# Optimization experiments

Measured on AMD Instinct MI355X. Metric: run time of the kernel, lower is better.

The kernel has to match this reference:

```python
import jax, jax.numpy as jnp
import numpy as np

N = 50000      # nodes
E = 800000     # edges (avg degree 16)
LM = 768       # lm_input_dim
H = 192        # hidden_dim = 32*6
B6 = 32        # per-branch dim = hidden_dim/6
SLOPE = 0.01   # nn.LeakyReLU default negative slope


def setup_inputs() -> dict:
    key = jax.random.key(0)
    ks = jax.random.split(key, 32)
    f = lambda i, shape, s=0.05: (jax.random.normal(ks[i], shape, jnp.float32) * s)
    inp = {
        "pre_x": f(0, (N, LM)),
        "x": f(1, (N, LM)),
        "edge_index": jax.random.randint(ks[2], (2, E), 0, N),
        "edge_type": jax.random.randint(ks[3], (E,), 0, 3),
        "num_prop": f(4, (N, 5)),
        "num_category": f(5, (N, 1)),
        "des_tensor": f(6, (N, LM)),
        "tweet_tensor": f(7, (N, LM)),
        # parameters (torch nn.Linear convention: W is [out, in], y = x @ W.T + b)
        "W_des": f(8, (B6, LM)), "b_des": f(9, (B6,)),
        "W_tweet": f(10, (B6, LM)), "b_tweet": f(11, (B6,)),
        "W_tweet_tr": f(12, (B6, LM)), "b_tweet_tr": f(13, (B6,)),
        "W_prop": f(14, (B6, 5)), "b_prop": f(15, (B6,)),
        "W_cat": f(16, (B6, 1)), "b_cat": f(17, (B6,)),
        "W_text": f(18, (B6, LM)), "b_text": f(19, (B6,)),
        "W_in": f(20, (H, H)), "b_in": f(21, (H,)),
        "W_c1": f(22, (H, H)), "b_c1": f(23, (H,)),
        "W_c2": f(24, (H, H)), "b_c2": f(25, (H,)),
        "W_o1": f(26, (96, H)), "b_o1": f(27, (96,)),
        "W_o2": f(28, (2, 96)), "b_o2": f(29, (2,)),
    }
    return inp


def _gcn_conv(h, W, b, src, dst):
    """PyG GCNConv: symmetric-normalized aggregation with added self-loops.
    out[v] = sum_{u->v} (d_u d_v)^{-1/2} (h_u W^T) + (1/d_v) (h_v W^T) + b
    where d includes the self-loop (+1)."""
    n = h.shape[0]
    hW = h @ W.T                                                  # [N, H]
    deg = jax.ops.segment_sum(jnp.ones(src.shape[0], h.dtype), dst,
                              num_segments=n) + 1.0               # [N]
    dinv = jax.lax.rsqrt(deg)
    norm = dinv[src] * dinv[dst]                                  # [E]
    agg = jax.ops.segment_sum(hW[src] * norm[:, None], dst,
                              num_segments=n)                     # [N, H]
    return agg + hW * (1.0 / deg)[:, None] + b


def reference(pre_x, x, edge_index, edge_type, num_prop, num_category,
              des_tensor, tweet_tensor,
              W_des, b_des, W_tweet, b_tweet, W_tweet_tr, b_tweet_tr,
              W_prop, b_prop, W_cat, b_cat, W_text, b_text,
              W_in, b_in, W_c1, b_c1, W_c2, b_c2,
              W_o1, b_o1, W_o2, b_o2):
    lrelu = lambda v: jax.nn.leaky_relu(v, SLOPE)
    branch = lambda t, W, b: lrelu(t @ W.T + b)   # dropout is identity in eval

    d = branch(des_tensor, W_des, b_des)
    pre_t = branch(pre_x, W_tweet, b_tweet)
    t = branch(x, W_tweet_tr, b_tweet_tr)
    n = branch(num_prop, W_prop, b_prop)
    c = branch(num_category, W_cat, b_cat)
    tw = branch(tweet_tensor, W_text, b_text)

    h = jnp.concatenate((n, c, d, tw, pre_t, t), axis=1)          # [N, 192]
    h = lrelu(h @ W_in.T + b_in)

    src, dst = edge_index[0], edge_index[1]
    h = _gcn_conv(h, W_c1, b_c1, src, dst)
    h = _gcn_conv(h, W_c2, b_c2, src, dst)

    em = lrelu(h @ W_o1.T + b_o1)                                 # [N, 96]
    out = em @ W_o2.T + b_o2                                      # [N, 2]
    return (out, em)
```

## Files before the change

kernel.cpp:

```cpp
#include <hip/hip_runtime.h>

#define NN 50000
#define EE 800000
#define LMD 768
#define HD 192
#define SLOPE 0.01f

typedef short bf16x8 __attribute__((ext_vector_type(8)));
typedef float f32x4 __attribute__((ext_vector_type(4)));
typedef unsigned short u16;

__device__ __forceinline__ float lrelu(float v){ return v > 0.f ? v : SLOPE * v; }

__device__ __forceinline__ u16 f2bf(float f){
    unsigned u = __float_as_uint(f);
    u += 0x7FFF + ((u >> 16) & 1u);
    return (u16)(u >> 16);
}
__device__ __forceinline__ float bf2f(u16 v){
    return __uint_as_float(((unsigned)v) << 16);
}

__global__ __launch_bounds__(256) void k_prep(
    const float* __restrict__ W0, const float* __restrict__ W1,
    const float* __restrict__ W2, const float* __restrict__ W3,
    const float* __restrict__ Win, const float* __restrict__ Wc1,
    const float* __restrict__ Wc2, const float* __restrict__ Wo1,
    u16* __restrict__ out)
{
    int m = blockIdx.y;
    int idx = blockIdx.x * 256 + threadIdx.x;
    const float* src; int nelem; int K;
    switch (m) {
      case 0: src = W0;  nelem = 32*768;  K = 768; break;
      case 1: src = W1;  nelem = 32*768;  K = 768; break;
      case 2: src = W2;  nelem = 32*768;  K = 768; break;
      case 3: src = W3;  nelem = 32*768;  K = 768; break;
      case 4: src = Win; nelem = 192*192; K = 192; break;
      case 5: src = Wc1; nelem = 192*192; K = 192; break;
      case 6: src = Wc2; nelem = 192*192; K = 192; break;
      default: src = Wo1; nelem = 96*192; K = 192; break;
    }
    if (idx >= nelem) return;
    u16 v = f2bf(src[idx]);
    int c = idx / K, k = idx - c * K;
    int cb = c >> 4, lr = c & 15;
    int sg = k >> 5, kk = k & 31, hi = kk >> 3, j = kk & 7;
    int lane = hi * 16 + lr;
    size_t dst;
    if (m < 4)      dst = (size_t)m * 24576 + (sg * 2 + cb) * 512 + lane * 8 + j;
    else if (m < 7) dst = 98304 + (size_t)(m - 4) * 36864 + (sg * 12 + cb) * 512 + lane * 8 + j;
    else            dst = 208896 + (size_t)(sg * 6 + cb) * 512 + lane * 8 + j;
    out[dst] = v;
}

__global__ __launch_bounds__(256) void k_branch(
    const float* __restrict__ des, const float* __restrict__ twt,
    const float* __restrict__ prex, const float* __restrict__ xx,
    const u16* __restrict__ Wf,
    const float* __restrict__ bd, const float* __restrict__ btx,
    const float* __restrict__ btw, const float* __restrict__ btr,
    u16* __restrict__ h)
{
    const int br = blockIdx.y;
    const float* A; const float* bias; int colBase;
    switch (br) {
      case 0:  A = des;  bias = bd;  colBase = 64;  break;
      case 1:  A = twt;  bias = btx; colBase = 96;  break;
      case 2:  A = prex; bias = btw; colBase = 128; break;
      default: A = xx;   bias = btr; colBase = 160; break;
    }
    const u16* Wb = Wf + br * 24576;

    const int t = threadIdx.x, w = t >> 6, l = t & 63;
    const int hi = l >> 4, lr = l & 15;
    const int rowBase = blockIdx.x * 64;
    int row = rowBase + w * 16 + lr;
    int rowc = row < NN ? row : NN - 1;
    const float4* ap = reinterpret_cast<const float4*>(A) + (size_t)rowc * 192;
    const int fo = hi * 2;

    f32x4 acc[2] = {};
    float4 buf[4][2];
    #pragma unroll
    for (int s = 0; s < 4; ++s) {
        buf[s][0] = ap[s * 8 + fo];
        buf[s][1] = ap[s * 8 + fo + 1];
    }

    #pragma unroll
    for (int sg = 0; sg < 24; ++sg) {
        float4 a0 = buf[sg & 3][0], a1 = buf[sg & 3][1];
        if (sg + 4 < 24) {
            buf[sg & 3][0] = ap[(sg + 4) * 8 + fo];
            buf[sg & 3][1] = ap[(sg + 4) * 8 + fo + 1];
        }
        bf16x8 af;
        af[0] = (short)f2bf(a0.x); af[1] = (short)f2bf(a0.y);
        af[2] = (short)f2bf(a0.z); af[3] = (short)f2bf(a0.w);
        af[4] = (short)f2bf(a1.x); af[5] = (short)f2bf(a1.y);
        af[6] = (short)f2bf(a1.z); af[7] = (short)f2bf(a1.w);
        #pragma unroll
        for (int cb = 0; cb < 2; ++cb) {
            bf16x8 bf = *reinterpret_cast<const bf16x8*>(Wb + (sg * 2 + cb) * 512 + l * 8);
            acc[cb] = __builtin_amdgcn_mfma_f32_16x16x32_bf16(af, bf, acc[cb], 0, 0, 0);
        }
    }

    #pragma unroll
    for (int cb = 0; cb < 2; ++cb) {
        int cl = cb * 16 + lr;
        float bv = bias[cl];
        #pragma unroll
        for (int rg = 0; rg < 4; ++rg) {
            int r = rowBase + w * 16 + hi * 4 + rg;
            if (r < NN)
                h[(size_t)r * HD + colBase + cl] = f2bf(lrelu(acc[cb][rg] + bv));
        }
    }
}

template<bool BIAS, bool LRELU>
__global__ __launch_bounds__(256) void k_hgemm(
    const u16* __restrict__ A, const u16* __restrict__ Wf,
    const float* __restrict__ bias, u16* __restrict__ out)
{
    const int t = threadIdx.x, w = t >> 6, l = t & 63;
    const int hi = l >> 4, lr = l & 15;
    const int rowBase = blockIdx.x * 64;
    int row = rowBase + w * 16 + lr;
    int rowc = row < NN ? row : NN - 1;
    const u16* ap = A + (size_t)rowc * HD;

    bf16x8 afr[6];
    #pragma unroll
    for (int sg = 0; sg < 6; ++sg)
        afr[sg] = *reinterpret_cast<const bf16x8*>(ap + sg * 32 + hi * 8);

    f32x4 acc[12] = {};
    #pragma unroll
    for (int sg = 0; sg < 6; ++sg) {
        #pragma unroll
        for (int cb = 0; cb < 12; ++cb) {
            bf16x8 bf = *reinterpret_cast<const bf16x8*>(Wf + (sg * 12 + cb) * 512 + l * 8);
            acc[cb] = __builtin_amdgcn_mfma_f32_16x16x32_bf16(afr[sg], bf, acc[cb], 0, 0, 0);
        }
    }

    #pragma unroll
    for (int cb = 0; cb < 12; ++cb) {
        int cl = cb * 16 + lr;
        float bv = BIAS ? bias[cl] : 0.f;
        #pragma unroll
        for (int rg = 0; rg < 4; ++rg) {
            int r = rowBase + w * 16 + hi * 4 + rg;
            if (r < NN) {
                float v = acc[cb][rg] + bv;
                if (LRELU) v = lrelu(v);
                out[(size_t)r * HD + cl] = f2bf(v);
            }
        }
    }
}

__global__ __launch_bounds__(256) void k_final(
    const u16* __restrict__ A, const u16* __restrict__ Wf,
    const float* __restrict__ b1, const float* __restrict__ W2,
    const float* __restrict__ b2, float* __restrict__ em, float* __restrict__ out)
{
    const int t = threadIdx.x, w = t >> 6, l = t & 63;
    const int hi = l >> 4, lr = l & 15;
    const int rowBase = blockIdx.x * 64;
    int row = rowBase + w * 16 + lr;
    int rowc = row < NN ? row : NN - 1;
    const u16* ap = A + (size_t)rowc * HD;

    bf16x8 afr[6];
    #pragma unroll
    for (int sg = 0; sg < 6; ++sg)
        afr[sg] = *reinterpret_cast<const bf16x8*>(ap + sg * 32 + hi * 8);

    f32x4 acc[6] = {};
    #pragma unroll
    for (int sg = 0; sg < 6; ++sg) {
        #pragma unroll
        for (int cb = 0; cb < 6; ++cb) {
            bf16x8 bf = *reinterpret_cast<const bf16x8*>(Wf + (sg * 6 + cb) * 512 + l * 8);
            acc[cb] = __builtin_amdgcn_mfma_f32_16x16x32_bf16(afr[sg], bf, acc[cb], 0, 0, 0);
        }
    }

    float w2v[2][6], bv[6];
    #pragma unroll
    for (int cb = 0; cb < 6; ++cb) {
        bv[cb] = b1[cb * 16 + lr];
        w2v[0][cb] = W2[cb * 16 + lr];
        w2v[1][cb] = W2[96 + cb * 16 + lr];
    }

    #pragma unroll
    for (int rg = 0; rg < 4; ++rg) {
        int r = rowBase + w * 16 + hi * 4 + rg;
        float o0 = 0.f, o1 = 0.f;
        #pragma unroll
        for (int cb = 0; cb < 6; ++cb) {
            float v = lrelu(acc[cb][rg] + bv[cb]);
            if (r < NN) em[(size_t)r * 96 + cb * 16 + lr] = v;
            o0 += v * w2v[0][cb];
            o1 += v * w2v[1][cb];
        }
        #pragma unroll
        for (int d = 1; d < 16; d <<= 1) {
            o0 += __shfl_xor(o0, d);
            o1 += __shfl_xor(o1, d);
        }
        if (lr == 0 && r < NN) {
            out[r * 2 + 0] = o0 + b2[0];
            out[r * 2 + 1] = o1 + b2[1];
        }
    }
}

__global__ __launch_bounds__(256) void k_small_branch(
    const float* __restrict__ nprop, const float* __restrict__ ncat,
    const float* __restrict__ Wp, const float* __restrict__ bp,
    const float* __restrict__ Wc, const float* __restrict__ bc,
    u16* __restrict__ h)
{
    int idx = blockIdx.x * 256 + threadIdx.x;
    if (idx >= NN * 64) return;
    int row = idx >> 6, c = idx & 63;
    float acc;
    if (c < 32) {
        acc = bp[c];
        #pragma unroll
        for (int k = 0; k < 5; ++k) acc += nprop[row * 5 + k] * Wp[c * 5 + k];
    } else {
        int cc = c - 32;
        acc = bc[cc] + ncat[row] * Wc[cc];
    }
    h[(size_t)row * HD + c] = f2bf(lrelu(acc));
}

__global__ void k_count(const int* __restrict__ ei, int* __restrict__ deg)
{
    int e = blockIdx.x * 256 + threadIdx.x;
    if (e < EE) atomicAdd(&deg[ei[EE + e]], 1);
}

__global__ void k_deginv(const int* __restrict__ deg, float* __restrict__ dinv, float* __restrict__ invdeg)
{
    int v = blockIdx.x * 256 + threadIdx.x;
    if (v < NN) {
        float d = (float)(deg[v] + 1);
        dinv[v] = rsqrtf(d);
        invdeg[v] = 1.0f / d;
    }
}

__global__ __launch_bounds__(1024) void k_scan1(const int* __restrict__ deg, int* __restrict__ rp, int* __restrict__ part)
{
    __shared__ int sh[1024];
    int tid = threadIdx.x, i = blockIdx.x * 1024 + tid;
    int x = (i < NN) ? deg[i] : 0;
    sh[tid] = x;
    __syncthreads();
    for (int off = 1; off < 1024; off <<= 1) {
        int y = (tid >= off) ? sh[tid - off] : 0;
        __syncthreads();
        sh[tid] += y;
        __syncthreads();
    }
    if (i < NN) rp[i] = sh[tid] - x;
    if (tid == 1023) part[blockIdx.x] = sh[tid];
}

__global__ void k_scan2(int* part, int nb, int* rp)
{
    if (threadIdx.x == 0 && blockIdx.x == 0) {
        int run = 0;
        for (int b = 0; b < nb; ++b) { int t = part[b]; part[b] = run; run += t; }
        rp[NN] = run;
    }
}

__global__ void k_scan3(int* rp, const int* __restrict__ part)
{
    int i = blockIdx.x * 256 + threadIdx.x;
    if (i < NN) rp[i] += part[i >> 10];
}

__global__ void k_fill(const int* __restrict__ ei, const float* __restrict__ dinv,
                       int* __restrict__ cursor, int* __restrict__ cs, float* __restrict__ nrm)
{
    int e = blockIdx.x * 256 + threadIdx.x;
    if (e >= EE) return;
    int s = ei[e], d = ei[EE + e];
    int pos = atomicAdd(&cursor[d], 1);
    cs[pos] = s;
    nrm[pos] = dinv[s] * dinv[d];
}

__global__ __launch_bounds__(240) void k_agg(const u16* __restrict__ hW,
    const int* __restrict__ rp, const int* __restrict__ cs, const float* __restrict__ nrm,
    const float* __restrict__ invdeg, const float* __restrict__ bias, u16* __restrict__ out)
{
    int v = blockIdx.x * 5 + threadIdx.y;
    int f0 = threadIdx.x * 4;
    int s0 = rp[v], s1 = rp[v + 1];
    float4 bv = *reinterpret_cast<const float4*>(bias + f0);
    ushort4 hv = *reinterpret_cast<const ushort4*>(hW + (size_t)v * HD + f0);
    float idg = invdeg[v];
    float a0 = bf2f(hv.x) * idg + bv.x;
    float a1 = bf2f(hv.y) * idg + bv.y;
    float a2 = bf2f(hv.z) * idg + bv.z;
    float a3 = bf2f(hv.w) * idg + bv.w;
    int i = s0;
    for (; i + 4 <= s1; i += 4) {
        int c0 = cs[i], c1 = cs[i+1], c2 = cs[i+2], c3 = cs[i+3];
        float n0 = nrm[i], n1 = nrm[i+1], n2 = nrm[i+2], n3 = nrm[i+3];
        ushort4 g0 = *reinterpret_cast<const ushort4*>(hW + (size_t)c0 * HD + f0);
        ushort4 g1 = *reinterpret_cast<const ushort4*>(hW + (size_t)c1 * HD + f0);
        ushort4 g2 = *reinterpret_cast<const ushort4*>(hW + (size_t)c2 * HD + f0);
        ushort4 g3 = *reinterpret_cast<const ushort4*>(hW + (size_t)c3 * HD + f0);
        a0 += bf2f(g0.x) * n0; a1 += bf2f(g0.y) * n0; a2 += bf2f(g0.z) * n0; a3 += bf2f(g0.w) * n0;
        a0 += bf2f(g1.x) * n1; a1 += bf2f(g1.y) * n1; a2 += bf2f(g1.z) * n1; a3 += bf2f(g1.w) * n1;
        a0 += bf2f(g2.x) * n2; a1 += bf2f(g2.y) * n2; a2 += bf2f(g2.z) * n2; a3 += bf2f(g2.w) * n2;
        a0 += bf2f(g3.x) * n3; a1 += bf2f(g3.y) * n3; a2 += bf2f(g3.z) * n3; a3 += bf2f(g3.w) * n3;
    }
    for (; i < s1; ++i) {
        int c = cs[i]; float n = nrm[i];
        ushort4 g = *reinterpret_cast<const ushort4*>(hW + (size_t)c * HD + f0);
        a0 += bf2f(g.x) * n; a1 += bf2f(g.y) * n; a2 += bf2f(g.z) * n; a3 += bf2f(g.w) * n;
    }
    ushort4 o;
    o.x = f2bf(a0); o.y = f2bf(a1); o.z = f2bf(a2); o.w = f2bf(a3);
    *reinterpret_cast<ushort4*>(out + (size_t)v * HD + f0) = o;
}

extern "C" void kernel_launch(void* const* d_in, const int* in_sizes, int n_in,
                              void* d_out, int out_size, void* d_ws, size_t ws_size,
                              hipStream_t stream)
{
    const float* pre_x = (const float*)d_in[0];
    const float* x     = (const float*)d_in[1];
    const int*   ei    = (const int*)d_in[2];
    const float* nprop = (const float*)d_in[4];
    const float* ncat  = (const float*)d_in[5];
    const float* des   = (const float*)d_in[6];
    const float* twt   = (const float*)d_in[7];
    const float* W_des  = (const float*)d_in[8],  *b_des  = (const float*)d_in[9];
    const float* W_tw   = (const float*)d_in[10], *b_tw   = (const float*)d_in[11];
    const float* W_tr   = (const float*)d_in[12], *b_tr   = (const float*)d_in[13];
    const float* W_prop = (const float*)d_in[14], *b_prop = (const float*)d_in[15];
    const float* W_cat  = (const float*)d_in[16], *b_cat  = (const float*)d_in[17];
    const float* W_text = (const float*)d_in[18], *b_text = (const float*)d_in[19];
    const float* W_in   = (const float*)d_in[20], *b_in   = (const float*)d_in[21];
    const float* W_c1   = (const float*)d_in[22], *b_c1   = (const float*)d_in[23];
    const float* W_c2   = (const float*)d_in[24], *b_c2   = (const float*)d_in[25];
    const float* W_o1   = (const float*)d_in[26], *b_o1   = (const float*)d_in[27];
    const float* W_o2   = (const float*)d_in[28], *b_o2   = (const float*)d_in[29];

    char* base = (char*)d_ws;
    size_t off = 0;
    auto alloc = [&](size_t bytes) -> char* {
        char* p = base + off;
        off = (off + bytes + 255) & ~(size_t)255;
        return p;
    };
    u16*   hA     = (u16*)alloc((size_t)NN * HD * 2);
    u16*   hB     = (u16*)alloc((size_t)NN * HD * 2);
    u16*   hC     = (u16*)alloc((size_t)NN * HD * 2);
    u16*   Wprep  = (u16*)alloc((size_t)227328 * 2);
    float* dinv   = (float*)alloc((size_t)NN * 4);
    float* invdeg = (float*)alloc((size_t)NN * 4);
    int*   deg    = (int*)alloc((size_t)NN * 4);
    int*   rp     = (int*)alloc((size_t)(NN + 1) * 4);
    int*   cursor = (int*)alloc((size_t)NN * 4);
    int*   part   = (int*)alloc(64 * 4);
    int*   cs     = (int*)alloc((size_t)EE * 4);
    float* nrm    = (float*)alloc((size_t)EE * 4);
    (void)ws_size; (void)in_sizes; (void)n_in; (void)out_size;

    float* outp = (float*)d_out;
    float* em   = outp + (size_t)NN * 2;

    const int rb    = (NN + 255) / 256;
    const int rb64  = (NN + 63) / 64;
    const int eb    = (EE + 255) / 256;
    const int nb1024 = (NN + 1023) / 1024;

    hipMemsetAsync(deg, 0, (size_t)NN * 4, stream);
    hipLaunchKernelGGL(k_prep, dim3(144, 8), dim3(256), 0, stream,
        W_des, W_text, W_tw, W_tr, W_in, W_c1, W_c2, W_o1, Wprep);
    hipLaunchKernelGGL(k_count,  dim3(eb), dim3(256), 0, stream, ei, deg);
    hipLaunchKernelGGL(k_deginv, dim3(rb), dim3(256), 0, stream, deg, dinv, invdeg);
    hipLaunchKernelGGL(k_scan1,  dim3(nb1024), dim3(1024), 0, stream, deg, rp, part);
    hipLaunchKernelGGL(k_scan2,  dim3(1), dim3(1), 0, stream, part, nb1024, rp);
    hipLaunchKernelGGL(k_scan3,  dim3(rb), dim3(256), 0, stream, rp, part);
    hipMemcpyAsync(cursor, rp, (size_t)NN * 4, hipMemcpyDeviceToDevice, stream);
    hipLaunchKernelGGL(k_fill,   dim3(eb), dim3(256), 0, stream, ei, dinv, cursor, cs, nrm);

    hipLaunchKernelGGL(k_branch, dim3(rb64, 4), dim3(256), 0, stream,
        des, twt, pre_x, x, Wprep, b_des, b_text, b_tw, b_tr, hA);
    hipLaunchKernelGGL(k_small_branch, dim3((NN * 64 + 255) / 256), dim3(256), 0, stream,
        nprop, ncat, W_prop, b_prop, W_cat, b_cat, hA);

    hipLaunchKernelGGL((k_hgemm<true, true>),   dim3(rb64), dim3(256), 0, stream,
        hA, Wprep + 98304, b_in, hB);
    hipLaunchKernelGGL((k_hgemm<false, false>), dim3(rb64), dim3(256), 0, stream,
        hB, Wprep + 98304 + 36864, nullptr, hC);
    hipLaunchKernelGGL(k_agg, dim3(NN / 5), dim3(48, 5), 0, stream, hC, rp, cs, nrm, invdeg, b_c1, hA);
    hipLaunchKernelGGL((k_hgemm<false, false>), dim3(rb64), dim3(256), 0, stream,
        hA, Wprep + 98304 + 2 * 36864, nullptr, hB);
    hipLaunchKernelGGL(k_agg, dim3(NN / 5), dim3(48, 5), 0, stream, hB, rp, cs, nrm, invdeg, b_c2, hC);

    hipLaunchKernelGGL(k_final, dim3(rb64), dim3(256), 0, stream,
        hC, Wprep + 208896, b_o1, W_o2, b_o2, em, outp);
}
```

Measured before the change: 440.5 us.

## Stage GEMM weights in LDS and coalesce branch activation loads via shared tiles

The branch GEMM now reads fp32 activation rows with fully coalesced per-row loads, converts them to bf16 and writes them into a swizzled shared tile. MFMA A-fragments are then read from that tile, while weight halves are staged into LDS and the global loads for the next chunk are software-pipelined against compute. The hidden-dim GEMMs and the final head now use 512-thread blocks covering 128 rows and copy the whole weight matrix into shared memory once per block, instead of each wave re-reading fragments from global/L2. This adds LDS pressure and barriers, which may lower occupancy, and the swizzle indexing has to be exactly right.

```diff
diff --git a/kernel.cpp b/kernel.cpp
--- a/kernel.cpp
+++ b/kernel.cpp
@@ -19,6 +19,9 @@
 }
 __device__ __forceinline__ float bf2f(u16 v){
     return __uint_as_float(((unsigned)v) << 16);
+}
+__device__ __forceinline__ bf16x8 as_bf8(float4 v){
+    union { float4 f; bf16x8 b; } u; u.f = v; return u.b;
 }
 
 __global__ __launch_bounds__(256) void k_prep(
@@ -54,6 +57,34 @@
     out[dst] = v;
 }
 
+#define BR_LOAD(R0, R1, c) { \
+  _Pragma("unroll") for (int rt = 0; rt < 4; ++rt) { \
+    const float* p_ = abase[rt] + (c) * 128; \
+    R0[rt] = *(const float4*)p_; R1[rt] = *(const float4*)(p_ + 4); } \
+  _Pragma("unroll") for (int rt = 0; rt < 4; ++rt) { \
+    asm volatile("" :: "v"(R0[rt].x), "v"(R0[rt].y), "v"(R0[rt].z), "v"(R0[rt].w)); \
+    asm volatile("" :: "v"(R1[rt].x), "v"(R1[rt].y), "v"(R1[rt].z), "v"(R1[rt].w)); } }
+
+#define BR_WRITE(R0, R1) { \
+  _Pragma("unroll") for (int rt = 0; rt < 4; ++rt) { \
+    uint4 pk_; \
+    pk_.x = (unsigned)f2bf(R0[rt].x) | ((unsigned)f2bf(R0[rt].y) << 16); \
+    pk_.y = (unsigned)f2bf(R0[rt].z) | ((unsigned)f2bf(R0[rt].w) << 16); \
+    pk_.z = (unsigned)f2bf(R1[rt].x) | ((unsigned)f2bf(R1[rt].y) << 16); \
+    pk_.w = (unsigned)f2bf(R1[rt].z) | ((unsigned)f2bf(R1[rt].w) << 16); \
+    *(uint4*)(Asg + wrIdx[rt]) = pk_; } }
+
+#define BR_COMPUTE(fb) { \
+  _Pragma("unroll") for (int sgl = 0; sgl < 4; ++sgl) { \
+    bf16x8 af_ = *(const bf16x8*)(Asg + wbase + sgl * 512 + rdOff); \
+    _Pragma("unroll") for (int cb = 0; cb < 2; ++cb) { \
+      bf16x8 bf_ = *(const bf16x8*)(Bs + (fb) + (sgl * 2 + cb) * 512 + l * 8); \
+      acc[cb] = __builtin_amdgcn_mfma_f32_16x16x32_bf16(af_, bf_, acc[cb], 0, 0, 0); } } }
+
+#define BR_STAGEB(half) { \
+  const uint4* s_ = (const uint4*)(Wb + (half) * 12288); uint4* d_ = (uint4*)Bs; \
+  _Pragma("unroll") for (int i = 0; i < 6; ++i) d_[i * 256 + t] = s_[i * 256 + t]; }
+
 __global__ __launch_bounds__(256) void k_branch(
     const float* __restrict__ des, const float* __restrict__ twt,
     const float* __restrict__ prex, const float* __restrict__ xx,
@@ -62,6 +93,8 @@
     const float* __restrict__ btw, const float* __restrict__ btr,
     u16* __restrict__ h)
 {
+    __shared__ u16 Bs[12288];
+    __shared__ u16 Asg[8192];
     const int br = blockIdx.y;
     const float* A; const float* bias; int colBase;
     switch (br) {
@@ -75,37 +108,40 @@
     const int t = threadIdx.x, w = t >> 6, l = t & 63;
     const int hi = l >> 4, lr = l & 15;
     const int rowBase = blockIdx.x * 64;
-    int row = rowBase + w * 16 + lr;
-    int rowc = row < NN ? row : NN - 1;
-    const float4* ap = reinterpret_cast<const float4*>(A) + (size_t)rowc * 192;
-    const int fo = hi * 2;
+    const int wbase = w * 2048;
+    const int rdOff = (l ^ hi) * 8;
+
+    const float* abase[4];
+    int wrIdx[4];
+    #pragma unroll
+    for (int rt = 0; rt < 4; ++rt) {
+        int r = rowBase + w * 16 + rt * 4 + hi;
+        if (r >= NN) r = NN - 1;
+        abase[rt] = A + (size_t)r * LMD + lr * 8;
+        int slot = ((l & 3) << 4) | (rt * 4 + hi);
+        wrIdx[rt] = wbase + (lr >> 2) * 512 + (slot ^ (l & 3)) * 8;
+    }
 
     f32x4 acc[2] = {};
-    float4 buf[4][2];
-    #pragma unroll
-    for (int s = 0; s < 4; ++s) {
-        buf[s][0] = ap[s * 8 + fo];
-        buf[s][1] = ap[s * 8 + fo + 1];
-    }
-
-    #pragma unroll
-    for (int sg = 0; sg < 24; ++sg) {
-        float4 a0 = buf[sg & 3][0], a1 = buf[sg & 3][1];
-        if (sg + 4 < 24) {
-            buf[sg & 3][0] = ap[(sg + 4) * 8 + fo];
-            buf[sg & 3][1] = ap[(sg + 4) * 8 + fo + 1];
-        }
-        bf16x8 af;
-        af[0] = (short)f2bf(a0.x); af[1] = (short)f2bf(a0.y);
-        af[2] = (short)f2bf(a0.z); af[3] = (short)f2bf(a0.w);
-        af[4] = (short)f2bf(a1.x); af[5] = (short)f2bf(a1.y);
-        af[6] = (short)f2bf(a1.z); af[7] = (short)f2bf(a1.w);
-        #pragma unroll
-        for (int cb = 0; cb < 2; ++cb) {
-            bf16x8 bf = *reinterpret_cast<const bf16x8*>(Wb + (sg * 2 + cb) * 512 + l * 8);
-            acc[cb] = __builtin_amdgcn_mfma_f32_16x16x32_bf16(af, bf, acc[cb], 0, 0, 0);
-        }
-    }
+    float4 a0[4], a1[4], b0[4], b1[4];
+
+    BR_LOAD(a0, a1, 0);
+    BR_STAGEB(0);
+    __syncthreads();
+    BR_LOAD(b0, b1, 1);
+    BR_WRITE(a0, a1);  BR_COMPUTE(0);
+    BR_LOAD(a0, a1, 2);
+    BR_WRITE(b0, b1);  BR_COMPUTE(4096);
+    BR_LOAD(b0, b1, 3);
+    BR_WRITE(a0, a1);  BR_COMPUTE(8192);
+    __syncthreads();
+    BR_STAGEB(1);
+    __syncthreads();
+    BR_LOAD(a0, a1, 4);
+    BR_WRITE(b0, b1);  BR_COMPUTE(0);
+    BR_LOAD(b0, b1, 5);
+    BR_WRITE(a0, a1);  BR_COMPUTE(4096);
+    BR_WRITE(b0, b1);  BR_COMPUTE(8192);
 
     #pragma unroll
     for (int cb = 0; cb < 2; ++cb) {
@@ -121,29 +157,38 @@
 }
 
 template<bool BIAS, bool LRELU>
-__global__ __launch_bounds__(256) void k_hgemm(
+__global__ __launch_bounds__(512) void k_hgemm(
     const u16* __restrict__ A, const u16* __restrict__ Wf,
     const float* __restrict__ bias, u16* __restrict__ out)
 {
+    __shared__ u16 Bs[36864];
     const int t = threadIdx.x, w = t >> 6, l = t & 63;
     const int hi = l >> 4, lr = l & 15;
-    const int rowBase = blockIdx.x * 64;
-    int row = rowBase + w * 16 + lr;
-    int rowc = row < NN ? row : NN - 1;
+    const int rowBase = blockIdx.x * 128;
+    {
+        const uint4* s_ = (const uint4*)Wf; uint4* d_ = (uint4*)Bs;
+        #pragma unroll
+        for (int i = 0; i < 9; ++i) d_[i * 512 + t] = s_[i * 512 + t];
+    }
+    int r0 = rowBase + w * 16 + lr;
+    int rowc = r0 < NN ? r0 : NN - 1;
     const u16* ap = A + (size_t)rowc * HD;
-
-    bf16x8 afr[6];
-    #pragma unroll
-    for (int sg = 0; sg < 6; ++sg)
-        afr[sg] = *reinterpret_cast<const bf16x8*>(ap + sg * 32 + hi * 8);
+    float4 araw[6];
+    #pragma unroll
+    for (int sg = 0; sg < 6; ++sg) {
+        araw[sg] = *(const float4*)(ap + sg * 32 + hi * 8);
+        asm volatile("" :: "v"(araw[sg].x), "v"(araw[sg].y), "v"(araw[sg].z), "v"(araw[sg].w));
+    }
+    __syncthreads();
 
     f32x4 acc[12] = {};
     #pragma unroll
     for (int sg = 0; sg < 6; ++sg) {
+        bf16x8 af = as_bf8(araw[sg]);
         #pragma unroll
         for (int cb = 0; cb < 12; ++cb) {
-            bf16x8 bf = *reinterpret_cast<const bf16x8*>(Wf + (sg * 12 + cb) * 512 + l * 8);
-            acc[cb] = __builtin_amdgcn_mfma_f32_16x16x32_bf16(afr[sg], bf, acc[cb], 0, 0, 0);
+            bf16x8 bf = *(const bf16x8*)(Bs + (sg * 12 + cb) * 512 + l * 8);
+            acc[cb] = __builtin_amdgcn_mfma_f32_16x16x32_bf16(af, bf, acc[cb], 0, 0, 0);
         }
     }
 
@@ -163,30 +208,39 @@
     }
 }
 
-__global__ __launch_bounds__(256) void k_final(
+__global__ __launch_bounds__(512) void k_final(
     const u16* __restrict__ A, const u16* __restrict__ Wf,
     const float* __restrict__ b1, const float* __restrict__ W2,
     const float* __restrict__ b2, float* __restrict__ em, float* __restrict__ out)
 {
+    __shared__ u16 Bs[18432];
     const int t = threadIdx.x, w = t >> 6, l = t & 63;
     const int hi = l >> 4, lr = l & 15;
-    const int rowBase = blockIdx.x * 64;
-    int row = rowBase + w * 16 + lr;
-    int rowc = row < NN ? row : NN - 1;
+    const int rowBase = blockIdx.x * 128;
+    {
+        const uint4* s_ = (const uint4*)Wf; uint4* d_ = (uint4*)Bs;
+        #pragma unroll
+        for (int i = 0; i < 5; ++i) { int idx = i * 512 + t; if (idx < 2304) d_[idx] = s_[idx]; }
+    }
+    int r0 = rowBase + w * 16 + lr;
+    int rowc = r0 < NN ? r0 : NN - 1;
     const u16* ap = A + (size_t)rowc * HD;
-
-    bf16x8 afr[6];
-    #pragma unroll
-    for (int sg = 0; sg < 6; ++sg)
-        afr[sg] = *reinterpret_cast<const bf16x8*>(ap + sg * 32 + hi * 8);
+    float4 araw[6];
+    #pragma unroll
+    for (int sg = 0; sg < 6; ++sg) {
+        araw[sg] = *(const float4*)(ap + sg * 32 + hi * 8);
+        asm volatile("" :: "v"(araw[sg].x), "v"(araw[sg].y), "v"(araw[sg].z), "v"(araw[sg].w));
+    }
+    __syncthreads();
 
     f32x4 acc[6] = {};
     #pragma unroll
     for (int sg = 0; sg < 6; ++sg) {
+        bf16x8 af = as_bf8(araw[sg]);
         #pragma unroll
         for (int cb = 0; cb < 6; ++cb) {
-            bf16x8 bf = *reinterpret_cast<const bf16x8*>(Wf + (sg * 6 + cb) * 512 + l * 8);
-            acc[cb] = __builtin_amdgcn_mfma_f32_16x16x32_bf16(afr[sg], bf, acc[cb], 0, 0, 0);
+            bf16x8 bf = *(const bf16x8*)(Bs + (sg * 6 + cb) * 512 + l * 8);
+            acc[cb] = __builtin_amdgcn_mfma_f32_16x16x32_bf16(af, bf, acc[cb], 0, 0, 0);
         }
     }
 
@@ -385,9 +439,10 @@
     float* outp = (float*)d_out;
     float* em   = outp + (size_t)NN * 2;
 
-    const int rb    = (NN + 255) / 256;
-    const int rb64  = (NN + 63) / 64;
-    const int eb    = (EE + 255) / 256;
+    const int rb     = (NN + 255) / 256;
+    const int rb64   = (NN + 63) / 64;
+    const int rb128  = (NN + 127) / 128;
+    const int eb     = (EE + 255) / 256;
     const int nb1024 = (NN + 1023) / 1024;
 
     hipMemsetAsync(deg, 0, (size_t)NN * 4, stream);
@@ -406,15 +461,15 @@
     hipLaunchKernelGGL(k_small_branch, dim3((NN * 64 + 255) / 256), dim3(256), 0, stream,
         nprop, ncat, W_prop, b_prop, W_cat, b_cat, hA);
 
-    hipLaunchKernelGGL((k_hgemm<true, true>),   dim3(rb64), dim3(256), 0, stream,
+    hipLaunchKernelGGL((k_hgemm<true, true>),   dim3(rb128), dim3(512), 0, stream,
         hA, Wprep + 98304, b_in, hB);
-    hipLaunchKernelGGL((k_hgemm<false, false>), dim3(rb64), dim3(256), 0, stream,
+    hipLaunchKernelGGL((k_hgemm<false, false>), dim3(rb128), dim3(512), 0, stream,
         hB, Wprep + 98304 + 36864, nullptr, hC);
     hipLaunchKernelGGL(k_agg, dim3(NN / 5), dim3(48, 5), 0, stream, hC, rp, cs, nrm, invdeg, b_c1, hA);
-    hipLaunchKernelGGL((k_hgemm<false, false>), dim3(rb64), dim3(256), 0, stream,
+    hipLaunchKernelGGL((k_hgemm<false, false>), dim3(rb128), dim3(512), 0, stream,
         hA, Wprep + 98304 + 2 * 36864, nullptr, hB);
     hipLaunchKernelGGL(k_agg, dim3(NN / 5), dim3(48, 5), 0, stream, hB, rp, cs, nrm, invdeg, b_c2, hC);
 
-    hipLaunchKernelGGL(k_final, dim3(rb64), dim3(256), 0, stream,
+    hipLaunchKernelGGL(k_final, dim3(rb128), dim3(512), 0, stream,
         hC, Wprep + 208896, b_o1, W_o2, b_o2, em, outp);
 }
```

Result: faster. 410.2 us (-6.9%).
